# Kernel optimization log

Hardware: AMD Instinct MI355X
Metric: run time of the kernel (lower is better)

Reference implementation:

```python
import jax, jax.numpy as jnp
import numpy as np

OBS_DIM = 256
FEAT = 128
HID = 64
N_OPT = 8
ACT_N = 18
B = 32768
TEMPERATURE = 1.0


def setup_inputs() -> dict:
    key = jax.random.key(0)
    ks = jax.random.split(key, 16)
    s = 0.05
    inp = {
        "obs": jax.random.normal(ks[0], (B, OBS_DIM), dtype=jnp.float32),
        "act": jax.random.randint(ks[1], (B,), 0, ACT_N, dtype=jnp.int32),
        "opt": jax.random.randint(ks[2], (B,), 0, N_OPT, dtype=jnp.int32),
        # feature trunk: obs_dim -> 64 -> 128, ReLU after both layers
        "fW1": jax.random.normal(ks[3], (HID, OBS_DIM), dtype=jnp.float32) * s,
        "fb1": jnp.zeros((HID,), dtype=jnp.float32),
        "fW2": jax.random.normal(ks[4], (FEAT, HID), dtype=jnp.float32) * s,
        "fb2": jnp.zeros((FEAT,), dtype=jnp.float32),
        # option policy / termination heads: 128 -> n_opts
        "pW": jax.random.normal(ks[5], (N_OPT, FEAT), dtype=jnp.float32) * s,
        "pb": jnp.zeros((N_OPT,), dtype=jnp.float32),
        "tW": jax.random.normal(ks[6], (N_OPT, FEAT), dtype=jnp.float32) * s,
        "tb": jnp.zeros((N_OPT,), dtype=jnp.float32),
        # per-option expert ensemble: 128 -> 64 -> act_n
        "oW1": jax.random.normal(ks[7], (N_OPT, HID, FEAT), dtype=jnp.float32) * s,
        "ob1": jnp.zeros((N_OPT, HID), dtype=jnp.float32),
        "oW2": jax.random.normal(ks[8], (N_OPT, ACT_N, HID), dtype=jnp.float32) * s,
        "ob2": jnp.zeros((N_OPT, ACT_N), dtype=jnp.float32),
    }
    return inp


def reference(obs, act, opt, fW1, fb1, fW2, fb2, pW, pb, tW, tb, oW1, ob1, oW2, ob2):
    # feature trunk (ReLU output activation as in mlp(..., output_activation=nn.ReLU))
    h = jax.nn.relu(obs @ fW1.T + fb1)          # [B, 64]
    state = jax.nn.relu(h @ fW2.T + fb2)        # [B, 128]

    # per-sample option-gathered expert MLP (vmap(fmodel) with params p[option])
    W1 = oW1[opt]                               # [B, 64, 128] irregular gather
    b1 = ob1[opt]                               # [B, 64]
    W2 = oW2[opt]                               # [B, act_n, 64]
    b2 = ob2[opt]                               # [B, act_n]
    eh = jax.nn.relu(jnp.einsum("bf,bhf->bh", state, W1) + b1)   # [B, 64]
    logits = jnp.einsum("bh,bah->ba", eh, W2) + b2               # [B, act_n]

    # Categorical(probs=softmax(logits / T)); log_prob(act) = log_softmax(logits/T)[act]
    logp_all = jax.nn.log_softmax(logits / TEMPERATURE, axis=-1)
    logp = jnp.take_along_axis(logp_all, act[:, None].astype(jnp.int32), axis=-1)[:, 0]

    # option value: take_along_dim(opt_dist, opt)
    opt_dist = state @ pW.T + pb                # [B, n_opts]
    optval = jnp.take_along_axis(opt_dist, opt[:, None].astype(jnp.int32), axis=-1)[:, 0]

    # termination prob: sigmoid(termination(state))[opt]
    term_dist = jax.nn.sigmoid(state @ tW.T + tb)
    termprob = jnp.take_along_axis(term_dist, opt[:, None].astype(jnp.int32), axis=-1)[:, 0]

    return (logp, optval, termprob)
```

## Files before the change

kernel.cpp:

```cpp
#include <hip/hip_runtime.h>
#include <hip/hip_bf16.h>
#include <math.h>

#define OBS_DIM 256
#define FEAT 128
#define HID 64
#define N_OPT 8
#define ACT_N 18
#define BATCH 32768

typedef unsigned short u16;
typedef unsigned int u32;
typedef __attribute__((ext_vector_type(8))) short short8;
typedef __attribute__((ext_vector_type(4))) float f32x4;
typedef __attribute__((ext_vector_type(4))) u16 u16x4;

#define MFMA(a, b, c) __builtin_amdgcn_mfma_f32_16x16x32_bf16((a), (b), (c), 0, 0, 0)

#define SWZ(row, off) ((off) ^ (((row) & 7) << 4))

#define WS_STATE   0
#define WS_FW1     (8388608)
#define WS_FW2     (WS_FW1 + 64*256*2)
#define WS_PW      (WS_FW2 + 128*64*2)
#define WS_TW      (WS_PW  + 16*128*2)
#define WS_OW1     (WS_TW  + 16*128*2)
#define WS_OW2     (WS_OW1 + 8*64*128*2)
#define WS_CNT     (WS_OW2 + 8*32*64*2)
#define WS_IDX     (WS_CNT + 128)

__device__ __forceinline__ u16 bf(float x) {
    u32 u = __float_as_uint(x);
    return (u16)((u + 0x7fffu + ((u >> 16) & 1u)) >> 16);
}

__global__ __launch_bounds__(256) void k_prep(
    const float* __restrict__ fW1, const float* __restrict__ fW2,
    const float* __restrict__ pW,  const float* __restrict__ tW,
    const float* __restrict__ oW1, const float* __restrict__ oW2,
    u16* __restrict__ fW1b, u16* __restrict__ fW2b,
    u16* __restrict__ pWb,  u16* __restrict__ tWb,
    u16* __restrict__ oW1b, u16* __restrict__ oW2b)
{
    int gid = blockIdx.x * 256 + threadIdx.x;
    int stride = gridDim.x * 256;
    for (int i = gid; i < 64 * 256; i += stride) fW1b[i] = bf(fW1[i]);
    for (int i = gid; i < 128 * 64; i += stride) fW2b[i] = bf(fW2[i]);
    for (int i = gid; i < 16 * 128; i += stride) {
        int r = i >> 7;
        pWb[i] = (r < 8) ? bf(pW[i]) : (u16)0;
        tWb[i] = (r < 8) ? bf(tW[i]) : (u16)0;
    }
    for (int i = gid; i < 8 * 64 * 128; i += stride) oW1b[i] = bf(oW1[i]);
    for (int i = gid; i < 8 * 32 * 64; i += stride) {
        int o = i >> 11, a = (i >> 6) & 31, e = i & 63;
        oW2b[i] = (a < ACT_N) ? bf(oW2[(o * ACT_N + a) * 64 + e]) : (u16)0;
    }
}

__global__ __launch_bounds__(256) void k_bucket(const int* __restrict__ opt,
                                                int* __restrict__ cnt,
                                                int* __restrict__ idx) {
    __shared__ int lcnt[N_OPT];
    __shared__ int lbase[N_OPT];
    int tid = threadIdx.x;
    if (tid < N_OPT) lcnt[tid] = 0;
    __syncthreads();
    int row = blockIdx.x * 256 + tid;
    int o = opt[row];
    int lpos = atomicAdd(&lcnt[o], 1);
    __syncthreads();
    if (tid < N_OPT) lbase[tid] = atomicAdd(&cnt[tid], lcnt[tid]);
    __syncthreads();
    idx[o * BATCH + lbase[o] + lpos] = row;
}

__global__ __launch_bounds__(256) void k_trunk(
    const float* __restrict__ obs, const int* __restrict__ opt,
    const u16* __restrict__ fW1b, const float* __restrict__ fb1,
    const u16* __restrict__ fW2b, const float* __restrict__ fb2,
    const u16* __restrict__ pWb,  const float* __restrict__ pb,
    const u16* __restrict__ tWb,  const float* __restrict__ tb,
    u16* __restrict__ state_g, float* __restrict__ out)
{
    __shared__ u16 lA[64 * 256];
    __shared__ u16 lH[64 * 64];
    __shared__ u16 lS[64 * 128];

    const int tid = threadIdx.x;
    const int tile = blockIdx.x;
    const int w = tid >> 6, l = tid & 63, lg = l >> 4, lc = l & 15;

    const float* op = obs + (size_t)tile * 64 * OBS_DIM;
    {
        char* lab = (char*)lA;
#pragma unroll
        for (int i = 0; i < 16; ++i) {
            int flat = tid * 4 + i * 1024;
            float4 v = *reinterpret_cast<const float4*>(op + flat);
            int row = flat >> 8, col = flat & 255;
            u16x4 u;
            u.x = bf(v.x); u.y = bf(v.y); u.z = bf(v.z); u.w = bf(v.w);
            *reinterpret_cast<u16x4*>(lab + row * 512 + SWZ(row, col * 2)) = u;
        }
    }
    __syncthreads();

    f32x4 acc1[4] = {{0.f,0.f,0.f,0.f},{0.f,0.f,0.f,0.f},{0.f,0.f,0.f,0.f},{0.f,0.f,0.f,0.f}};
    {
        const int arow = 16 * w + lc;
        const char* lab = (const char*)lA;
#pragma unroll
        for (int ks = 0; ks < 8; ++ks) {
            short8 a = *reinterpret_cast<const short8*>(lab + arow * 512 + SWZ(arow, ks * 64 + lg * 16));
#pragma unroll
            for (int nn = 0; nn < 4; ++nn) {
                short8 b = *reinterpret_cast<const short8*>(fW1b + (nn * 16 + lc) * 256 + ks * 32 + lg * 8);
                acc1[nn] = MFMA(a, b, acc1[nn]);
            }
        }
    }
#pragma unroll
    for (int nn = 0; nn < 4; ++nn) {
        int col = nn * 16 + lc;
        float bias = fb1[col];
#pragma unroll
        for (int r = 0; r < 4; ++r) {
            int row = 16 * w + 4 * lg + r;
            *(u16*)((char*)lH + row * 128 + SWZ(row, col * 2)) = bf(fmaxf(acc1[nn][r] + bias, 0.f));
        }
    }
    __syncthreads();

    f32x4 acc2[8];
#pragma unroll
    for (int nn = 0; nn < 8; ++nn) acc2[nn] = (f32x4){0.f,0.f,0.f,0.f};
    {
        const int arow = 16 * w + lc;
        const char* lhb = (const char*)lH;
#pragma unroll
        for (int ks = 0; ks < 2; ++ks) {
            short8 a = *reinterpret_cast<const short8*>(lhb + arow * 128 + SWZ(arow, ks * 64 + lg * 16));
#pragma unroll
            for (int nn = 0; nn < 8; ++nn) {
                short8 b = *reinterpret_cast<const short8*>(fW2b + (nn * 16 + lc) * 64 + ks * 32 + lg * 8);
                acc2[nn] = MFMA(a, b, acc2[nn]);
            }
        }
    }
#pragma unroll
    for (int nn = 0; nn < 8; ++nn) {
        int col = nn * 16 + lc;
        float bias = fb2[col];
#pragma unroll
        for (int r = 0; r < 4; ++r) {
            int row = 16 * w + 4 * lg + r;
            *(u16*)((char*)lS + row * 256 + SWZ(row, col * 2)) = bf(fmaxf(acc2[nn][r] + bias, 0.f));
        }
    }
    __syncthreads();

    {
        int row = tid >> 2, q = tid & 3;
        char* dst = (char*)(state_g + ((size_t)tile * 64 + row) * FEAT);
#pragma unroll
        for (int u = 0; u < 4; ++u) {
            short8 v = *reinterpret_cast<const short8*>((char*)lS + row * 256 + SWZ(row, q * 64 + u * 16));
            *reinterpret_cast<short8*>(dst + q * 64 + u * 16) = v;
        }
    }

    f32x4 accP = {0.f,0.f,0.f,0.f}, accT = {0.f,0.f,0.f,0.f};
    {
        const int arow = 16 * w + lc;
        const char* lsb = (const char*)lS;
#pragma unroll
        for (int ks = 0; ks < 4; ++ks) {
            short8 a = *reinterpret_cast<const short8*>(lsb + arow * 256 + SWZ(arow, ks * 64 + lg * 16));
            short8 bp = *reinterpret_cast<const short8*>(pWb + lc * 128 + ks * 32 + lg * 8);
            short8 bt = *reinterpret_cast<const short8*>(tWb + lc * 128 + ks * 32 + lg * 8);
            accP = MFMA(a, bp, accP);
            accT = MFMA(a, bt, accT);
        }
    }
#pragma unroll
    for (int r = 0; r < 4; ++r) {
        int row = 16 * w + 4 * lg + r;
        int grow = tile * 64 + row;
        int o = opt[grow];
        float pv = __shfl(accP[r], (l & 48) | o, 64);
        float tv = __shfl(accT[r], (l & 48) | o, 64);
        if (lc == 0) {
            out[BATCH + grow] = pv + pb[o];
            out[2 * BATCH + grow] = 1.f / (1.f + expf(-(tv + tb[o])));
        }
    }
}

__global__ __launch_bounds__(256) void k_expert(
    const u16* __restrict__ state_g, const int* __restrict__ cnt,
    const int* __restrict__ idx, const int* __restrict__ act,
    const u16* __restrict__ oW1b, const float* __restrict__ ob1,
    const u16* __restrict__ oW2b, const float* __restrict__ ob2,
    float* __restrict__ out)
{
    __shared__ u16 lS[64 * 128];
    __shared__ u16 lE[64 * 64];
    __shared__ float lL[64 * 19];

    const int tid = threadIdx.x;
    const int o = blockIdx.x & 7, c0 = blockIdx.x >> 3;
    const int n = cnt[o];
    const int ntiles = (n + 63) >> 6;
    const u16* W1 = oW1b + o * HID * FEAT;
    const u16* W2 = oW2b + o * 32 * HID;
    const float* b1 = ob1 + o * HID;
    const float* b2 = ob2 + o * ACT_N;
    const int w = tid >> 6, l = tid & 63, lg = l >> 4, lc = l & 15;

    for (int t = c0; t < ntiles; t += 64) {
        {
            int lrow = tid >> 2, q = tid & 3;
            int i = t * 64 + lrow;
            int grow = (i < n) ? idx[o * BATCH + i] : -1;
#pragma unroll
            for (int u = 0; u < 4; ++u) {
                short8 v;
                if (grow >= 0)
                    v = *reinterpret_cast<const short8*>((const char*)(state_g + (size_t)grow * FEAT) + q * 64 + u * 16);
                else
                    v = (short8)0;
                *reinterpret_cast<short8*>((char*)lS + lrow * 256 + SWZ(lrow, q * 64 + u * 16)) = v;
            }
        }
        __syncthreads();

        f32x4 acc[4];
#pragma unroll
        for (int nn = 0; nn < 4; ++nn) acc[nn] = (f32x4){0.f,0.f,0.f,0.f};
        {
            const int arow = 16 * w + lc;
            const char* lsb = (const char*)lS;
#pragma unroll
            for (int ks = 0; ks < 4; ++ks) {
                short8 a = *reinterpret_cast<const short8*>(lsb + arow * 256 + SWZ(arow, ks * 64 + lg * 16));
#pragma unroll
                for (int nn = 0; nn < 4; ++nn) {
                    short8 b = *reinterpret_cast<const short8*>(W1 + (nn * 16 + lc) * 128 + ks * 32 + lg * 8);
                    acc[nn] = MFMA(a, b, acc[nn]);
                }
            }
        }
#pragma unroll
        for (int nn = 0; nn < 4; ++nn) {
            int col = nn * 16 + lc;
            float bias = b1[col];
#pragma unroll
            for (int r = 0; r < 4; ++r) {
                int row = 16 * w + 4 * lg + r;
                *(u16*)((char*)lE + row * 128 + SWZ(row, col * 2)) = bf(fmaxf(acc[nn][r] + bias, 0.f));
            }
        }
        __syncthreads();

        f32x4 acc2[2];
        acc2[0] = (f32x4){0.f,0.f,0.f,0.f};
        acc2[1] = (f32x4){0.f,0.f,0.f,0.f};
        {
            const int arow = 16 * w + lc;
            const char* leb = (const char*)lE;
#pragma unroll
            for (int ks = 0; ks < 2; ++ks) {
                short8 a = *reinterpret_cast<const short8*>(leb + arow * 128 + SWZ(arow, ks * 64 + lg * 16));
#pragma unroll
                for (int nn = 0; nn < 2; ++nn) {
                    short8 b = *reinterpret_cast<const short8*>(W2 + (nn * 16 + lc) * 64 + ks * 32 + lg * 8);
                    acc2[nn] = MFMA(a, b, acc2[nn]);
                }
            }
        }
#pragma unroll
        for (int nn = 0; nn < 2; ++nn) {
            int col = nn * 16 + lc;
            if (col < ACT_N) {
                float bias = b2[col];
#pragma unroll
                for (int r = 0; r < 4; ++r) {
                    int row = 16 * w + 4 * lg + r;
                    lL[row * 19 + col] = acc2[nn][r] + bias;
                }
            }
        }
        __syncthreads();

        if (tid < 64) {
            int i = t * 64 + tid;
            if (i < n) {
                int grow = idx[o * BATCH + i];
                const float* lr = &lL[tid * 19];
                float mx = lr[0];
#pragma unroll
                for (int a = 1; a < ACT_N; ++a) mx = fmaxf(mx, lr[a]);
                float s = 0.f;
#pragma unroll
                for (int a = 0; a < ACT_N; ++a) s += expf(lr[a] - mx);
                int aa = act[grow];
                out[grow] = (lr[aa] - mx) - logf(s);
            }
        }
        __syncthreads();
    }
}

extern "C" void kernel_launch(void* const* d_in, const int* in_sizes, int n_in,
                              void* d_out, int out_size, void* d_ws, size_t ws_size,
                              hipStream_t stream) {
    const float* obs = (const float*)d_in[0];
    const int*   act = (const int*)d_in[1];
    const int*   opt = (const int*)d_in[2];
    const float* fW1 = (const float*)d_in[3];
    const float* fb1 = (const float*)d_in[4];
    const float* fW2 = (const float*)d_in[5];
    const float* fb2 = (const float*)d_in[6];
    const float* pW  = (const float*)d_in[7];
    const float* pb  = (const float*)d_in[8];
    const float* tW  = (const float*)d_in[9];
    const float* tb  = (const float*)d_in[10];
    const float* oW1 = (const float*)d_in[11];
    const float* ob1 = (const float*)d_in[12];
    const float* oW2 = (const float*)d_in[13];
    const float* ob2 = (const float*)d_in[14];
    float* out = (float*)d_out;

    char* ws = (char*)d_ws;
    u16* state_g = (u16*)(ws + WS_STATE);
    u16* fW1b = (u16*)(ws + WS_FW1);
    u16* fW2b = (u16*)(ws + WS_FW2);
    u16* pWb  = (u16*)(ws + WS_PW);
    u16* tWb  = (u16*)(ws + WS_TW);
    u16* oW1b = (u16*)(ws + WS_OW1);
    u16* oW2b = (u16*)(ws + WS_OW2);
    int* cnt  = (int*)(ws + WS_CNT);
    int* idx  = (int*)(ws + WS_IDX);

    hipMemsetAsync(cnt, 0, N_OPT * sizeof(int), stream);
    k_prep<<<64, 256, 0, stream>>>(fW1, fW2, pW, tW, oW1, oW2,
                                   fW1b, fW2b, pWb, tWb, oW1b, oW2b);
    k_bucket<<<BATCH / 256, 256, 0, stream>>>(opt, cnt, idx);
    k_trunk<<<BATCH / 64, 256, 0, stream>>>(obs, opt, fW1b, fb1, fW2b, fb2,
                                            pWb, pb, tWb, tb, state_g, out);
    k_expert<<<512, 256, 0, stream>>>(state_g, cnt, idx, act,
                                      oW1b, ob1, oW2b, ob2, out);
}
```

Baseline: 134.6 us.

## Fuse trunk and expert MLP into one kernel computing all options per tile

Merges the trunk, head and expert kernels into a single per-tile kernel and drops the bucketing pass and the global state buffer. Each tile evaluates all eight expert MLPs on its rows with MFMA and keeps only the rows matching each row's option, so no gather or sort is needed. This removes two launches, a memset, the state round trip through global memory and the indirect gathers. In exchange it does roughly eight times the expert matmul work, and the softmax reduction is spread across four lanes per row.

Measured after the change: 152.9 us. +13.6%, slower.

```diff
diff --git a/kernel.cpp b/kernel.cpp
--- a/kernel.cpp
+++ b/kernel.cpp
@@ -19,15 +19,12 @@
 
 #define SWZ(row, off) ((off) ^ (((row) & 7) << 4))
 
-#define WS_STATE   0
-#define WS_FW1     (8388608)
-#define WS_FW2     (WS_FW1 + 64*256*2)
-#define WS_PW      (WS_FW2 + 128*64*2)
-#define WS_TW      (WS_PW  + 16*128*2)
-#define WS_OW1     (WS_TW  + 16*128*2)
-#define WS_OW2     (WS_OW1 + 8*64*128*2)
-#define WS_CNT     (WS_OW2 + 8*32*64*2)
-#define WS_IDX     (WS_CNT + 128)
+#define WS_FW1 0
+#define WS_FW2 (WS_FW1 + 64*256*2)
+#define WS_PW  (WS_FW2 + 128*64*2)
+#define WS_TW  (WS_PW  + 16*128*2)
+#define WS_OW1 (WS_TW  + 16*128*2)
+#define WS_OW2 (WS_OW1 + 8*64*128*2)
 
 __device__ __forceinline__ u16 bf(float x) {
     u32 u = __float_as_uint(x);
@@ -58,42 +55,32 @@
     }
 }
 
-__global__ __launch_bounds__(256) void k_bucket(const int* __restrict__ opt,
-                                                int* __restrict__ cnt,
-                                                int* __restrict__ idx) {
-    __shared__ int lcnt[N_OPT];
-    __shared__ int lbase[N_OPT];
-    int tid = threadIdx.x;
-    if (tid < N_OPT) lcnt[tid] = 0;
-    __syncthreads();
-    int row = blockIdx.x * 256 + tid;
-    int o = opt[row];
-    int lpos = atomicAdd(&lcnt[o], 1);
-    __syncthreads();
-    if (tid < N_OPT) lbase[tid] = atomicAdd(&cnt[tid], lcnt[tid]);
-    __syncthreads();
-    idx[o * BATCH + lbase[o] + lpos] = row;
-}
-
-__global__ __launch_bounds__(256) void k_trunk(
+__global__ __launch_bounds__(256) void k_fused(
     const float* __restrict__ obs, const int* __restrict__ opt,
+    const int* __restrict__ act,
     const u16* __restrict__ fW1b, const float* __restrict__ fb1,
     const u16* __restrict__ fW2b, const float* __restrict__ fb2,
     const u16* __restrict__ pWb,  const float* __restrict__ pb,
     const u16* __restrict__ tWb,  const float* __restrict__ tb,
-    u16* __restrict__ state_g, float* __restrict__ out)
+    const u16* __restrict__ oW1b, const float* __restrict__ ob1,
+    const u16* __restrict__ oW2b, const float* __restrict__ ob2,
+    float* __restrict__ out)
 {
-    __shared__ u16 lA[64 * 256];
-    __shared__ u16 lH[64 * 64];
-    __shared__ u16 lS[64 * 128];
+    __shared__ char lmem[40 * 1024];
+    __shared__ int lOpt[64];
+    char* lA = lmem;
+    char* lH = lmem + 32 * 1024;
+    char* lS = lmem;
+    char* lE = lmem + 16 * 1024;
+    float* lL = (float*)(lmem + 24 * 1024);
 
     const int tid = threadIdx.x;
     const int tile = blockIdx.x;
     const int w = tid >> 6, l = tid & 63, lg = l >> 4, lc = l & 15;
-
-    const float* op = obs + (size_t)tile * 64 * OBS_DIM;
-    {
-        char* lab = (char*)lA;
+    const int arow = 16 * w + lc;
+
+    {
+        const float* op = obs + (size_t)tile * 64 * OBS_DIM;
 #pragma unroll
         for (int i = 0; i < 16; ++i) {
             int flat = tid * 4 + i * 1024;
@@ -101,214 +88,173 @@
             int row = flat >> 8, col = flat & 255;
             u16x4 u;
             u.x = bf(v.x); u.y = bf(v.y); u.z = bf(v.z); u.w = bf(v.w);
-            *reinterpret_cast<u16x4*>(lab + row * 512 + SWZ(row, col * 2)) = u;
-        }
-    }
-    __syncthreads();
-
-    f32x4 acc1[4] = {{0.f,0.f,0.f,0.f},{0.f,0.f,0.f,0.f},{0.f,0.f,0.f,0.f},{0.f,0.f,0.f,0.f}};
-    {
-        const int arow = 16 * w + lc;
-        const char* lab = (const char*)lA;
+            *reinterpret_cast<u16x4*>(lA + row * 512 + SWZ(row, col * 2)) = u;
+        }
+        if (tid < 64) lOpt[tid] = opt[tile * 64 + tid];
+    }
+    __syncthreads();
+
+    {
+        f32x4 acc1[4] = {{0,0,0,0},{0,0,0,0},{0,0,0,0},{0,0,0,0}};
 #pragma unroll
         for (int ks = 0; ks < 8; ++ks) {
-            short8 a = *reinterpret_cast<const short8*>(lab + arow * 512 + SWZ(arow, ks * 64 + lg * 16));
+            short8 a = *reinterpret_cast<const short8*>(lA + arow * 512 + SWZ(arow, ks * 64 + lg * 16));
 #pragma unroll
             for (int nn = 0; nn < 4; ++nn) {
                 short8 b = *reinterpret_cast<const short8*>(fW1b + (nn * 16 + lc) * 256 + ks * 32 + lg * 8);
                 acc1[nn] = MFMA(a, b, acc1[nn]);
             }
         }
-    }
-#pragma unroll
-    for (int nn = 0; nn < 4; ++nn) {
-        int col = nn * 16 + lc;
-        float bias = fb1[col];
-#pragma unroll
-        for (int r = 0; r < 4; ++r) {
-            int row = 16 * w + 4 * lg + r;
-            *(u16*)((char*)lH + row * 128 + SWZ(row, col * 2)) = bf(fmaxf(acc1[nn][r] + bias, 0.f));
-        }
-    }
-    __syncthreads();
-
-    f32x4 acc2[8];
-#pragma unroll
-    for (int nn = 0; nn < 8; ++nn) acc2[nn] = (f32x4){0.f,0.f,0.f,0.f};
-    {
-        const int arow = 16 * w + lc;
-        const char* lhb = (const char*)lH;
+#pragma unroll
+        for (int nn = 0; nn < 4; ++nn) {
+            int col = nn * 16 + lc;
+            float bias = fb1[col];
+#pragma unroll
+            for (int r = 0; r < 4; ++r) {
+                int row = 16 * w + 4 * lg + r;
+                *(u16*)(lH + row * 128 + SWZ(row, col * 2)) = bf(fmaxf(acc1[nn][r] + bias, 0.f));
+            }
+        }
+    }
+    __syncthreads();
+
+    {
+        f32x4 acc2[8];
+#pragma unroll
+        for (int nn = 0; nn < 8; ++nn) acc2[nn] = (f32x4){0,0,0,0};
 #pragma unroll
         for (int ks = 0; ks < 2; ++ks) {
-            short8 a = *reinterpret_cast<const short8*>(lhb + arow * 128 + SWZ(arow, ks * 64 + lg * 16));
+            short8 a = *reinterpret_cast<const short8*>(lH + arow * 128 + SWZ(arow, ks * 64 + lg * 16));
 #pragma unroll
             for (int nn = 0; nn < 8; ++nn) {
                 short8 b = *reinterpret_cast<const short8*>(fW2b + (nn * 16 + lc) * 64 + ks * 32 + lg * 8);
                 acc2[nn] = MFMA(a, b, acc2[nn]);
             }
         }
-    }
-#pragma unroll
-    for (int nn = 0; nn < 8; ++nn) {
-        int col = nn * 16 + lc;
-        float bias = fb2[col];
-#pragma unroll
-        for (int r = 0; r < 4; ++r) {
-            int row = 16 * w + 4 * lg + r;
-            *(u16*)((char*)lS + row * 256 + SWZ(row, col * 2)) = bf(fmaxf(acc2[nn][r] + bias, 0.f));
-        }
-    }
-    __syncthreads();
-
-    {
-        int row = tid >> 2, q = tid & 3;
-        char* dst = (char*)(state_g + ((size_t)tile * 64 + row) * FEAT);
-#pragma unroll
-        for (int u = 0; u < 4; ++u) {
-            short8 v = *reinterpret_cast<const short8*>((char*)lS + row * 256 + SWZ(row, q * 64 + u * 16));
-            *reinterpret_cast<short8*>(dst + q * 64 + u * 16) = v;
-        }
-    }
-
-    f32x4 accP = {0.f,0.f,0.f,0.f}, accT = {0.f,0.f,0.f,0.f};
-    {
-        const int arow = 16 * w + lc;
-        const char* lsb = (const char*)lS;
+#pragma unroll
+        for (int nn = 0; nn < 8; ++nn) {
+            int col = nn * 16 + lc;
+            float bias = fb2[col];
+#pragma unroll
+            for (int r = 0; r < 4; ++r) {
+                int row = 16 * w + 4 * lg + r;
+                *(u16*)(lS + row * 256 + SWZ(row, col * 2)) = bf(fmaxf(acc2[nn][r] + bias, 0.f));
+            }
+        }
+    }
+    __syncthreads();
+
+    int ro[4];
+#pragma unroll
+    for (int r = 0; r < 4; ++r) ro[r] = lOpt[16 * w + 4 * lg + r];
+
+    {
+        f32x4 accP = {0,0,0,0}, accT = {0,0,0,0};
 #pragma unroll
         for (int ks = 0; ks < 4; ++ks) {
-            short8 a = *reinterpret_cast<const short8*>(lsb + arow * 256 + SWZ(arow, ks * 64 + lg * 16));
+            short8 a = *reinterpret_cast<const short8*>(lS + arow * 256 + SWZ(arow, ks * 64 + lg * 16));
             short8 bp = *reinterpret_cast<const short8*>(pWb + lc * 128 + ks * 32 + lg * 8);
             short8 bt = *reinterpret_cast<const short8*>(tWb + lc * 128 + ks * 32 + lg * 8);
             accP = MFMA(a, bp, accP);
             accT = MFMA(a, bt, accT);
         }
-    }
-#pragma unroll
-    for (int r = 0; r < 4; ++r) {
-        int row = 16 * w + 4 * lg + r;
-        int grow = tile * 64 + row;
-        int o = opt[grow];
-        float pv = __shfl(accP[r], (l & 48) | o, 64);
-        float tv = __shfl(accT[r], (l & 48) | o, 64);
-        if (lc == 0) {
-            out[BATCH + grow] = pv + pb[o];
-            out[2 * BATCH + grow] = 1.f / (1.f + expf(-(tv + tb[o])));
-        }
-    }
-}
-
-__global__ __launch_bounds__(256) void k_expert(
-    const u16* __restrict__ state_g, const int* __restrict__ cnt,
-    const int* __restrict__ idx, const int* __restrict__ act,
-    const u16* __restrict__ oW1b, const float* __restrict__ ob1,
-    const u16* __restrict__ oW2b, const float* __restrict__ ob2,
-    float* __restrict__ out)
-{
-    __shared__ u16 lS[64 * 128];
-    __shared__ u16 lE[64 * 64];
-    __shared__ float lL[64 * 19];
-
-    const int tid = threadIdx.x;
-    const int o = blockIdx.x & 7, c0 = blockIdx.x >> 3;
-    const int n = cnt[o];
-    const int ntiles = (n + 63) >> 6;
-    const u16* W1 = oW1b + o * HID * FEAT;
-    const u16* W2 = oW2b + o * 32 * HID;
-    const float* b1 = ob1 + o * HID;
-    const float* b2 = ob2 + o * ACT_N;
-    const int w = tid >> 6, l = tid & 63, lg = l >> 4, lc = l & 15;
-
-    for (int t = c0; t < ntiles; t += 64) {
-        {
-            int lrow = tid >> 2, q = tid & 3;
-            int i = t * 64 + lrow;
-            int grow = (i < n) ? idx[o * BATCH + i] : -1;
-#pragma unroll
-            for (int u = 0; u < 4; ++u) {
-                short8 v;
-                if (grow >= 0)
-                    v = *reinterpret_cast<const short8*>((const char*)(state_g + (size_t)grow * FEAT) + q * 64 + u * 16);
-                else
-                    v = (short8)0;
-                *reinterpret_cast<short8*>((char*)lS + lrow * 256 + SWZ(lrow, q * 64 + u * 16)) = v;
-            }
-        }
-        __syncthreads();
-
-        f32x4 acc[4];
-#pragma unroll
-        for (int nn = 0; nn < 4; ++nn) acc[nn] = (f32x4){0.f,0.f,0.f,0.f};
-        {
-            const int arow = 16 * w + lc;
-            const char* lsb = (const char*)lS;
+#pragma unroll
+        for (int r = 0; r < 4; ++r) {
+            int grow = tile * 64 + 16 * w + 4 * lg + r;
+            int o = ro[r];
+            float pv = __shfl(accP[r], (l & 48) | o, 64);
+            float tv = __shfl(accT[r], (l & 48) | o, 64);
+            if (lc == 0) {
+                out[BATCH + grow] = pv + pb[o];
+                out[2 * BATCH + grow] = 1.f / (1.f + expf(-(tv + tb[o])));
+            }
+        }
+    }
+
+    {
+        short8 a4[4];
+#pragma unroll
+        for (int ks = 0; ks < 4; ++ks)
+            a4[ks] = *reinterpret_cast<const short8*>(lS + arow * 256 + SWZ(arow, ks * 64 + lg * 16));
+#pragma unroll
+        for (int o = 0; o < N_OPT; ++o) {
+            const u16* W1 = oW1b + o * HID * FEAT;
+            f32x4 acc[4] = {{0,0,0,0},{0,0,0,0},{0,0,0,0},{0,0,0,0}};
 #pragma unroll
             for (int ks = 0; ks < 4; ++ks) {
-                short8 a = *reinterpret_cast<const short8*>(lsb + arow * 256 + SWZ(arow, ks * 64 + lg * 16));
 #pragma unroll
                 for (int nn = 0; nn < 4; ++nn) {
                     short8 b = *reinterpret_cast<const short8*>(W1 + (nn * 16 + lc) * 128 + ks * 32 + lg * 8);
-                    acc[nn] = MFMA(a, b, acc[nn]);
-                }
-            }
-        }
-#pragma unroll
-        for (int nn = 0; nn < 4; ++nn) {
-            int col = nn * 16 + lc;
-            float bias = b1[col];
-#pragma unroll
-            for (int r = 0; r < 4; ++r) {
-                int row = 16 * w + 4 * lg + r;
-                *(u16*)((char*)lE + row * 128 + SWZ(row, col * 2)) = bf(fmaxf(acc[nn][r] + bias, 0.f));
-            }
-        }
-        __syncthreads();
-
-        f32x4 acc2[2];
-        acc2[0] = (f32x4){0.f,0.f,0.f,0.f};
-        acc2[1] = (f32x4){0.f,0.f,0.f,0.f};
-        {
-            const int arow = 16 * w + lc;
-            const char* leb = (const char*)lE;
+                    acc[nn] = MFMA(a4[ks], b, acc[nn]);
+                }
+            }
+#pragma unroll
+            for (int nn = 0; nn < 4; ++nn) {
+                int col = nn * 16 + lc;
+                float bias = ob1[o * HID + col];
+#pragma unroll
+                for (int r = 0; r < 4; ++r) {
+                    if (ro[r] == o) {
+                        int row = 16 * w + 4 * lg + r;
+                        *(u16*)(lE + row * 128 + SWZ(row, col * 2)) = bf(fmaxf(acc[nn][r] + bias, 0.f));
+                    }
+                }
+            }
+        }
+    }
+    __syncthreads();
+
+    {
+        short8 a2[2];
+#pragma unroll
+        for (int ks = 0; ks < 2; ++ks)
+            a2[ks] = *reinterpret_cast<const short8*>(lE + arow * 128 + SWZ(arow, ks * 64 + lg * 16));
+#pragma unroll
+        for (int o = 0; o < N_OPT; ++o) {
+            const u16* W2 = oW2b + o * 32 * HID;
+            f32x4 acc2[2] = {{0,0,0,0},{0,0,0,0}};
 #pragma unroll
             for (int ks = 0; ks < 2; ++ks) {
-                short8 a = *reinterpret_cast<const short8*>(leb + arow * 128 + SWZ(arow, ks * 64 + lg * 16));
 #pragma unroll
                 for (int nn = 0; nn < 2; ++nn) {
                     short8 b = *reinterpret_cast<const short8*>(W2 + (nn * 16 + lc) * 64 + ks * 32 + lg * 8);
-                    acc2[nn] = MFMA(a, b, acc2[nn]);
-                }
-            }
-        }
-#pragma unroll
-        for (int nn = 0; nn < 2; ++nn) {
-            int col = nn * 16 + lc;
-            if (col < ACT_N) {
-                float bias = b2[col];
-#pragma unroll
-                for (int r = 0; r < 4; ++r) {
-                    int row = 16 * w + 4 * lg + r;
-                    lL[row * 19 + col] = acc2[nn][r] + bias;
-                }
-            }
-        }
-        __syncthreads();
-
-        if (tid < 64) {
-            int i = t * 64 + tid;
-            if (i < n) {
-                int grow = idx[o * BATCH + i];
-                const float* lr = &lL[tid * 19];
-                float mx = lr[0];
-#pragma unroll
-                for (int a = 1; a < ACT_N; ++a) mx = fmaxf(mx, lr[a]);
-                float s = 0.f;
-#pragma unroll
-                for (int a = 0; a < ACT_N; ++a) s += expf(lr[a] - mx);
-                int aa = act[grow];
-                out[grow] = (lr[aa] - mx) - logf(s);
-            }
-        }
-        __syncthreads();
+                    acc2[nn] = MFMA(a2[ks], b, acc2[nn]);
+                }
+            }
+#pragma unroll
+            for (int nn = 0; nn < 2; ++nn) {
+                int col = nn * 16 + lc;
+                if (col < ACT_N) {
+                    float bias = ob2[o * ACT_N + col];
+#pragma unroll
+                    for (int r = 0; r < 4; ++r) {
+                        if (ro[r] == o) {
+                            int row = 16 * w + 4 * lg + r;
+                            lL[row * 19 + col] = acc2[nn][r] + bias;
+                        }
+                    }
+                }
+            }
+        }
+    }
+    __syncthreads();
+
+    {
+        int row = tid >> 2, q = tid & 3;
+        int grow = tile * 64 + row;
+        const float* lr = lL + row * 19;
+        float mx = -1e30f;
+        for (int a = q; a < ACT_N; a += 4) mx = fmaxf(mx, lr[a]);
+        mx = fmaxf(mx, __shfl_xor(mx, 1, 64));
+        mx = fmaxf(mx, __shfl_xor(mx, 2, 64));
+        float s = 0.f;
+        for (int a = q; a < ACT_N; a += 4) s += expf(lr[a] - mx);
+        s += __shfl_xor(s, 1, 64);
+        s += __shfl_xor(s, 2, 64);
+        if (q == 0) {
+            int aa = act[grow];
+            out[grow] = (lr[aa] - mx) - logf(s);
+        }
     }
 }
 
@@ -333,22 +279,17 @@
     float* out = (float*)d_out;
 
     char* ws = (char*)d_ws;
-    u16* state_g = (u16*)(ws + WS_STATE);
     u16* fW1b = (u16*)(ws + WS_FW1);
     u16* fW2b = (u16*)(ws + WS_FW2);
     u16* pWb  = (u16*)(ws + WS_PW);
     u16* tWb  = (u16*)(ws + WS_TW);
     u16* oW1b = (u16*)(ws + WS_OW1);
     u16* oW2b = (u16*)(ws + WS_OW2);
-    int* cnt  = (int*)(ws + WS_CNT);
-    int* idx  = (int*)(ws + WS_IDX);
-
-    hipMemsetAsync(cnt, 0, N_OPT * sizeof(int), stream);
+
     k_prep<<<64, 256, 0, stream>>>(fW1, fW2, pW, tW, oW1, oW2,
                                    fW1b, fW2b, pWb, tWb, oW1b, oW2b);
-    k_bucket<<<BATCH / 256, 256, 0, stream>>>(opt, cnt, idx);
-    k_trunk<<<BATCH / 64, 256, 0, stream>>>(obs, opt, fW1b, fb1, fW2b, fb2,
-                                            pWb, pb, tWb, tb, state_g, out);
-    k_expert<<<512, 256, 0, stream>>>(state_g, cnt, idx, act,
-                                      oW1b, ob1, oW2b, ob2, out);
-}
+    k_fused<<<BATCH / 64, 256, 0, stream>>>(obs, opt, act,
+                                            fW1b, fb1, fW2b, fb2,
+                                            pWb, pb, tWb, tb,
+                                            oW1b, ob1, oW2b, ob2, out);
+}
```
